# Optimization experiments

Hardware: AMD Instinct MI355X
Metric: run time of the kernel (lower is better)

## Reference

```python
import jax, jax.numpy as jnp
import numpy as np

B, SC, SV = 32, 300, 300
D, H, L, E, F = 512, 8, 6, 6, 1024
SEM = 768
VF = SEM + 1 + 1 + 6  # semantic + scene_offset + motion + emotion(6) = 776
CHORD, ROOT, ATTR = 159, 14, 14


def _ln(x, g, b, eps=1e-5):
    m = x.mean(-1, keepdims=True)
    v = ((x - m) ** 2).mean(-1, keepdims=True)
    return (x - m) / jnp.sqrt(v + eps) * g + b


def _mha(q_in, kv_in, qkv_w, qkv_b, ow, ob, mask=None):
    d = q_in.shape[-1]
    hd = d // H
    q = (q_in @ qkv_w[:d].T + qkv_b[:d]).reshape(q_in.shape[0], q_in.shape[1], H, hd)
    k = (kv_in @ qkv_w[d:2 * d].T + qkv_b[d:2 * d]).reshape(kv_in.shape[0], kv_in.shape[1], H, hd)
    v = (kv_in @ qkv_w[2 * d:].T + qkv_b[2 * d:]).reshape(kv_in.shape[0], kv_in.shape[1], H, hd)
    s = jnp.einsum('bqhd,bkhd->bhqk', q, k) / jnp.sqrt(jnp.asarray(hd, q.dtype))
    if mask is not None:
        s = s + mask
    a = jax.nn.softmax(s, axis=-1)
    o = jnp.einsum('bhqk,bkhd->bqhd', a, v).reshape(q_in.shape)
    return o @ ow.T + ob


def _moe(x, gw, gb, w1, b1, w2, b2, w3, b3):
    # top-2 routing over E experts, SwiGLU experts (GLUExpert)
    probs = jax.nn.softmax(x @ gw.T + gb, axis=-1)  # [B,S,E]
    topv, topi = jax.lax.top_k(probs, 2)
    wts = topv / topv.sum(-1, keepdims=True)
    full = (jax.nn.one_hot(topi, E, dtype=x.dtype) * wts[..., None]).sum(-2)  # [B,S,E]
    h = jax.nn.silu(jnp.einsum('bsd,edf->bsef', x, w1) + b1) * (jnp.einsum('bsd,edf->bsef', x, w2) + b2)
    eo = jnp.einsum('bsef,efd->bsed', h, w3) + b3
    return jnp.einsum('bse,bsed->bsd', full, eo)


def reference(x, x_root, x_attr, fsem, fkey, fscene, fmotion, femotion, emb_root, emb_attr, w_chord, b_chord, w_vis, b_vis, pos_c, pos_v, enc_qkv_w, enc_qkv_b, enc_ow, enc_ob, enc_ln1_g, enc_ln1_b, enc_ln2_g, enc_ln2_b, enc_gw, enc_gb, enc_w1, enc_b1, enc_w2, enc_b2, enc_w3, enc_b3, enc_fg, enc_fb, dec_sqkv_w, dec_sqkv_b, dec_sow, dec_sob, dec_cqkv_w, dec_cqkv_b, dec_cow, dec_cob, dec_ln1_g, dec_ln1_b, dec_ln2_g, dec_ln2_b, dec_ln3_g, dec_ln3_b, dec_gw, dec_gb, dec_w1, dec_b1, dec_w2, dec_b2, dec_w3, dec_b3, dec_fg, dec_fb, wout, bout):
    Bq, S = x_root.shape
    xe = emb_root[x_root] + emb_attr[x_attr]  # chord root + attr embeddings
    keyp = jnp.broadcast_to(fkey[:, 0][:, None, None], (Bq, S, 1)).astype(xe.dtype)
    xf = jnp.concatenate([xe, keyp], -1) @ w_chord.T + b_chord
    vfc = jnp.concatenate([fsem, fscene[..., None], fmotion[..., None], femotion], -1)  # [B,Sv,VF]
    vf = vfc @ w_vis.T + b_vis
    xf = xf + pos_c[:S][None]
    vf = vf + pos_v[:vf.shape[1]][None]
    causal = jnp.where(jnp.tril(jnp.ones((S, S), bool)), 0.0, jnp.finfo(xf.dtype).min).astype(xf.dtype)
    # encoder (post-norm): self-attn -> add&norm -> MoE -> add&norm
    h = vf
    for i in range(L):
        a = _mha(h, h, enc_qkv_w[i], enc_qkv_b[i], enc_ow[i], enc_ob[i])
        h = _ln(h + a, enc_ln1_g[i], enc_ln1_b[i])
        m = _moe(h, enc_gw[i], enc_gb[i], enc_w1[i], enc_b1[i], enc_w2[i], enc_b2[i], enc_w3[i], enc_b3[i])
        h = _ln(h + m, enc_ln2_g[i], enc_ln2_b[i])
    mem = _ln(h, enc_fg, enc_fb)
    # decoder: masked self-attn, cross-attn, MoE, each add&norm
    h = xf
    for i in range(L):
        a = _mha(h, h, dec_sqkv_w[i], dec_sqkv_b[i], dec_sow[i], dec_sob[i], causal)
        h = _ln(h + a, dec_ln1_g[i], dec_ln1_b[i])
        c = _mha(h, mem, dec_cqkv_w[i], dec_cqkv_b[i], dec_cow[i], dec_cob[i])
        h = _ln(h + c, dec_ln2_g[i], dec_ln2_b[i])
        m = _moe(h, dec_gw[i], dec_gb[i], dec_w1[i], dec_b1[i], dec_w2[i], dec_b2[i], dec_w3[i], dec_b3[i])
        h = _ln(h + m, dec_ln3_g[i], dec_ln3_b[i])
    h = _ln(h, dec_fg, dec_fb)
    return h @ wout.T + bout


def setup_inputs():
    key = jax.random.key(0)
    ks = iter(jax.random.split(key, 256))
    def nrm(*s):
        return jax.random.normal(next(ks), s, jnp.float32) * 0.02
    d = {}
    d['x'] = jax.random.randint(next(ks), (B, SC), 0, CHORD)
    d['x_root'] = jax.random.randint(next(ks), (B, SC), 0, ROOT)
    d['x_attr'] = jax.random.randint(next(ks), (B, SC), 0, ATTR)
    d['fsem'] = jax.random.normal(next(ks), (B, SV, SEM), jnp.float32)
    d['fkey'] = jax.random.uniform(next(ks), (B, 1), jnp.float32)
    d['fscene'] = jax.random.uniform(next(ks), (B, SV), jnp.float32)
    d['fmotion'] = jax.random.uniform(next(ks), (B, SV), jnp.float32)
    d['femotion'] = jax.random.uniform(next(ks), (B, SV, 6), jnp.float32)
    d['emb_root'] = nrm(ROOT, D)
    d['emb_attr'] = nrm(ATTR, D)
    d['w_chord'] = nrm(D, D + 1)
    d['b_chord'] = jnp.zeros((D,), jnp.float32)
    d['w_vis'] = nrm(D, VF)
    d['b_vis'] = jnp.zeros((D,), jnp.float32)
    d['pos_c'] = nrm(SC, D)
    d['pos_v'] = nrm(SV, D)
    def attn_params(pfx_qkv, pfx_o):
        d[pfx_qkv + '_w'] = nrm(L, 3 * D, D)
        d[pfx_qkv + '_b'] = jnp.zeros((L, 3 * D), jnp.float32)
        d[pfx_o + 'w'] = nrm(L, D, D)
        d[pfx_o + 'b'] = jnp.zeros((L, D), jnp.float32)
    attn_params('enc_qkv', 'enc_o')
    attn_params('dec_sqkv', 'dec_so')
    attn_params('dec_cqkv', 'dec_co')
    def moe_params(pfx):
        d[pfx + 'gw'] = nrm(L, E, D)
        d[pfx + 'gb'] = jnp.zeros((L, E), jnp.float32)
        d[pfx + 'w1'] = nrm(L, E, D, F)
        d[pfx + 'b1'] = jnp.zeros((L, E, F), jnp.float32)
        d[pfx + 'w2'] = nrm(L, E, D, F)
        d[pfx + 'b2'] = jnp.zeros((L, E, F), jnp.float32)
        d[pfx + 'w3'] = nrm(L, E, F, D)
        d[pfx + 'b3'] = jnp.zeros((L, E, D), jnp.float32)
    moe_params('enc_')
    moe_params('dec_')
    for n in ['enc_ln1', 'enc_ln2', 'dec_ln1', 'dec_ln2', 'dec_ln3']:
        d[n + '_g'] = jnp.ones((L, D), jnp.float32)
        d[n + '_b'] = jnp.zeros((L, D), jnp.float32)
    d['enc_fg'] = jnp.ones((D,), jnp.float32)
    d['enc_fb'] = jnp.zeros((D,), jnp.float32)
    d['dec_fg'] = jnp.ones((D,), jnp.float32)
    d['dec_fb'] = jnp.zeros((D,), jnp.float32)
    d['wout'] = nrm(CHORD, D)
    d['bout'] = jnp.zeros((CHORD,), jnp.float32)
    return d
```

## Files before the change

### kernel.cpp

```cpp
#include <hip/hip_runtime.h>

constexpr int B_ = 32, S_ = 300, D_ = 512, H_ = 8;
constexpr int L_ = 6, E_ = 6, F_ = 1024;
constexpr int CHORD_ = 159;
constexpr int R_ = B_ * S_;
constexpr int TD_ = 3 * D_;
constexpr int MT2_ = R_ / 128;
constexpr size_t WSCAP_ = (size_t)E_ * F_ * 512;

typedef short bfrag __attribute__((ext_vector_type(8)));
typedef float facc  __attribute__((ext_vector_type(4)));

static __device__ __forceinline__ facc mfma_(bfrag a, bfrag b, facc c) {
    return __builtin_amdgcn_mfma_f32_16x16x32_bf16(a, b, c, 0, 0, 0);
}

static __device__ __forceinline__ short f2bf_rne(float f) {
    unsigned u = __float_as_uint(f);
    return (short)((u + 0x7FFFu + ((u >> 16) & 1u)) >> 16);
}
static __device__ __forceinline__ void split2(float x, short& hi, short& lo) {
    unsigned u = __float_as_uint(x);
    hi = (short)(u >> 16);
    float fh = __uint_as_float(u & 0xFFFF0000u);
    lo = f2bf_rne(x - fh);
}

static __device__ __forceinline__ float2 blockReduce2(float s, float ss) {
    __shared__ float red[4][2];
    #pragma unroll
    for (int o = 32; o > 0; o >>= 1) { s += __shfl_down(s, o); ss += __shfl_down(ss, o); }
    const int wid = threadIdx.x >> 6, lane = threadIdx.x & 63;
    if (lane == 0) { red[wid][0] = s; red[wid][1] = ss; }
    __syncthreads();
    if (threadIdx.x == 0) {
        for (int w = 1; w < 4; ++w) { s += red[w][0]; ss += red[w][1]; }
        red[0][0] = s; red[0][1] = ss;
    }
    __syncthreads();
    return make_float2(red[0][0], red[0][1]);
}

__global__ void wsplit_kern(const float* __restrict__ src, short* __restrict__ dh, short* __restrict__ dl,
                            int N, int K, int Kp)
{
    const int idx = blockIdx.x * 256 + threadIdx.x;
    if (idx >= N * Kp) return;
    const int n = idx / Kp, k = idx - n * Kp;
    const float v = (k < K) ? src[(size_t)n * K + k] : 0.f;
    short sh, sl; split2(v, sh, sl);
    dh[idx] = sh; dl[idx] = sl;
}

__global__ __launch_bounds__(256) void tsplit_kern(const float* __restrict__ src,
                                                   short* __restrict__ dh, short* __restrict__ dl,
                                                   int K, int N)
{
    __shared__ float tile[32][33];
    const size_t eo = (size_t)blockIdx.z * K * N;
    const float* s = src + eo;
    short* oh = dh + eo;
    short* ol = dl + eo;
    const int kb = blockIdx.x * 32, nb = blockIdx.y * 32;
    const int c = threadIdx.x & 31, r0 = threadIdx.x >> 5;
    #pragma unroll
    for (int p = 0; p < 4; ++p) {
        const int r = r0 + p * 8;
        tile[r][c] = s[(size_t)(kb + r) * N + nb + c];
    }
    __syncthreads();
    #pragma unroll
    for (int p = 0; p < 4; ++p) {
        const int wn = r0 + p * 8;
        const float v = tile[c][wn];
        short sh, sl; split2(v, sh, sl);
        const size_t o = (size_t)(nb + wn) * K + kb + c;
        oh[o] = sh; ol[o] = sl;
    }
}

__global__ __launch_bounds__(256) void gemm_mfma(
    const short* __restrict__ Xh, const short* __restrict__ Xl,
    const short* __restrict__ Wh, const short* __restrict__ Wl, int Kp,
    const float* __restrict__ bias, const float* __restrict__ pos,
    float* __restrict__ Y, int ldy, int N,
    short* __restrict__ Yh, short* __restrict__ Yl)
{
    __shared__ __align__(16) short Ah[128][40], Al[128][40];
    __shared__ __align__(16) short Bh[128][40], Bl[128][40];
    const int m0 = blockIdx.x * 128, n0 = blockIdx.y * 128;
    const int tid = threadIdx.x;
    const int w = tid >> 6, l = tid & 63;
    const int wr = (w >> 1) * 64, wc = (w & 1) * 64;
    const facc zero = {0.f, 0.f, 0.f, 0.f};
    facc acc[4][4];
    #pragma unroll
    for (int i = 0; i < 4; ++i)
        #pragma unroll
        for (int j = 0; j < 4; ++j) acc[i][j] = zero;
    const int ar = tid >> 2, aks = (tid & 3) * 8;
    const int bc = tid >> 1, bk = (tid & 1) * 16;
    const bool bok = (n0 + bc) < N;
    const size_t a0 = (size_t)(m0 + ar) * Kp + aks;
    const size_t a1 = a0 + (size_t)64 * Kp;
    const size_t b0 = (size_t)(n0 + bc) * Kp + bk;
    const bfrag zf = {0, 0, 0, 0, 0, 0, 0, 0};
    bfrag pa0h, pa0l, pa1h, pa1l, pb0h, pb0l, pb1h, pb1l;
    auto LOAD = [&](int kc) {
        pa0h = *(const bfrag*)&Xh[a0 + kc];
        pa0l = *(const bfrag*)&Xl[a0 + kc];
        pa1h = *(const bfrag*)&Xh[a1 + kc];
        pa1l = *(const bfrag*)&Xl[a1 + kc];
        if (bok) {
            pb0h = *(const bfrag*)&Wh[b0 + kc];
            pb0l = *(const bfrag*)&Wl[b0 + kc];
            pb1h = *(const bfrag*)&Wh[b0 + kc + 8];
            pb1l = *(const bfrag*)&Wl[b0 + kc + 8];
        } else { pb0h = zf; pb0l = zf; pb1h = zf; pb1l = zf; }
    };
    LOAD(0);
    for (int kc = 0; kc < Kp; kc += 32) {
        *(bfrag*)&Ah[ar][aks]      = pa0h;  *(bfrag*)&Al[ar][aks]      = pa0l;
        *(bfrag*)&Ah[ar + 64][aks] = pa1h;  *(bfrag*)&Al[ar + 64][aks] = pa1l;
        *(bfrag*)&Bh[bc][bk]       = pb0h;  *(bfrag*)&Bl[bc][bk]       = pb0l;
        *(bfrag*)&Bh[bc][bk + 8]   = pb1h;  *(bfrag*)&Bl[bc][bk + 8]   = pb1l;
        __syncthreads();
        if (kc + 32 < Kp) LOAD(kc + 32);
        bfrag ah[4], al[4];
        #pragma unroll
        for (int i2 = 0; i2 < 4; ++i2) {
            ah[i2] = *(const bfrag*)&Ah[wr + i2 * 16 + (l & 15)][(l >> 4) * 8];
            al[i2] = *(const bfrag*)&Al[wr + i2 * 16 + (l & 15)][(l >> 4) * 8];
        }
        #pragma unroll
        for (int j = 0; j < 4; ++j) {
            const int cc = wc + j * 16 + (l & 15);
            const bfrag bh = *(const bfrag*)&Bh[cc][(l >> 4) * 8];
            const bfrag bl = *(const bfrag*)&Bl[cc][(l >> 4) * 8];
            #pragma unroll
            for (int i2 = 0; i2 < 4; ++i2) {
                acc[i2][j] = mfma_(ah[i2], bh, acc[i2][j]);
                acc[i2][j] = mfma_(al[i2], bh, acc[i2][j]);
                acc[i2][j] = mfma_(ah[i2], bl, acc[i2][j]);
            }
        }
        __syncthreads();
    }
    #pragma unroll
    for (int i2 = 0; i2 < 4; ++i2) {
        #pragma unroll
        for (int r = 0; r < 4; ++r) {
            const int m = m0 + wr + i2 * 16 + (l >> 4) * 4 + r;
            #pragma unroll
            for (int j = 0; j < 4; ++j) {
                const int n = n0 + wc + j * 16 + (l & 15);
                if (n < N) {
                    float y = acc[i2][j][r];
                    if (bias) y += bias[n];
                    if (pos)  y += pos[(size_t)(m % S_) * N + n];
                    Y[(size_t)m * ldy + n] = y;
                    if (Yh) {
                        short sh, sl; split2(y, sh, sl);
                        Yh[(size_t)m * ldy + n] = sh;
                        Yl[(size_t)m * ldy + n] = sl;
                    }
                }
            }
        }
    }
}

template<bool CAUSAL>
__global__ __launch_bounds__(320) void attn_kern(const float* __restrict__ qkv,
                                                 short* __restrict__ oh, short* __restrict__ ol)
{
    __shared__ float Ks[64][64];
    __shared__ float Vs[64][64];
    const int b = blockIdx.x >> 3, hh = blockIdx.x & 7;
    const int tid = threadIdx.x;
    const float* base = qkv + (size_t)b * S_ * TD_ + hh * 64;
    const bool act = tid < S_;
    float4 q4[16];
    if (act) {
        const float4* qp = (const float4*)(base + (size_t)tid * TD_);
        #pragma unroll
        for (int dd = 0; dd < 16; ++dd) q4[dd] = qp[dd];
    }
    float m = -3.0e38f, lsum = 0.f;
    float acc[64];
    #pragma unroll
    for (int d = 0; d < 64; ++d) acc[d] = 0.f;
    for (int j0 = 0; j0 < S_; j0 += 64) {
        const int tn = min(64, S_ - j0);
        __syncthreads();
        for (int idx = tid; idx < 64 * 64; idx += 320) {
            const int jj = idx >> 6, d = idx & 63;
            const bool ok = jj < tn;
            Ks[jj][d] = ok ? base[(size_t)(j0 + jj) * TD_ + D_ + d] : 0.f;
            Vs[jj][d] = ok ? base[(size_t)(j0 + jj) * TD_ + 2 * D_ + d] : 0.f;
        }
        __syncthreads();
        if (act) {
            const int jmax = CAUSAL ? min(tn, tid - j0 + 1) : tn;
            for (int jj = 0; jj < jmax; ++jj) {
                const float4* kp = (const float4*)Ks[jj];
                float s = 0.f;
                #pragma unroll
                for (int dd = 0; dd < 16; ++dd) {
                    const float4 kv = kp[dd];
                    s += q4[dd].x * kv.x + q4[dd].y * kv.y + q4[dd].z * kv.z + q4[dd].w * kv.w;
                }
                s *= 0.125f;
                float p;
                if (s > m) {
                    const float r = __expf(m - s);
                    lsum *= r;
                    #pragma unroll
                    for (int d = 0; d < 64; ++d) acc[d] *= r;
                    m = s; p = 1.f;
                } else {
                    p = __expf(s - m);
                }
                lsum += p;
                const float4* vp = (const float4*)Vs[jj];
                #pragma unroll
                for (int dd = 0; dd < 16; ++dd) {
                    const float4 vv = vp[dd];
                    acc[dd * 4 + 0] += p * vv.x; acc[dd * 4 + 1] += p * vv.y;
                    acc[dd * 4 + 2] += p * vv.z; acc[dd * 4 + 3] += p * vv.w;
                }
            }
        }
    }
    if (act) {
        const float inv = 1.f / lsum;
        const size_t ob = (size_t)(b * S_ + tid) * D_ + hh * 64;
        #pragma unroll
        for (int d = 0; d < 64; ++d) {
            short sh, sl; split2(acc[d] * inv, sh, sl);
            oh[ob + d] = sh; ol[ob + d] = sl;
        }
    }
}

__global__ __launch_bounds__(256) void add_ln_kern(float* __restrict__ h, const float* __restrict__ a,
    const float* __restrict__ g, const float* __restrict__ bb,
    short* __restrict__ dh, short* __restrict__ dl)
{
    const int r = blockIdx.x, tid = threadIdx.x;
    const size_t off = (size_t)r * D_;
    const float x0 = h[off + tid] + a[off + tid];
    const float x1 = h[off + tid + 256] + a[off + tid + 256];
    const float2 red = blockReduce2(x0 + x1, x0 * x0 + x1 * x1);
    const float mean = red.x * (1.f / D_);
    const float var = red.y * (1.f / D_) - mean * mean;
    const float rs = rsqrtf(var + 1e-5f);
    const float y0 = (x0 - mean) * rs * g[tid] + bb[tid];
    const float y1 = (x1 - mean) * rs * g[tid + 256] + bb[tid + 256];
    h[off + tid] = y0; h[off + tid + 256] = y1;
    short sh, sl;
    split2(y0, sh, sl); dh[off + tid] = sh;       dl[off + tid] = sl;
    split2(y1, sh, sl); dh[off + tid + 256] = sh; dl[off + tid + 256] = sl;
}

__global__ __launch_bounds__(256) void add2_ln_kern(float* __restrict__ h, const float* __restrict__ moeout,
    const float* __restrict__ g, const float* __restrict__ bb,
    short* __restrict__ dh, short* __restrict__ dl)
{
    const int r = blockIdx.x, tid = threadIdx.x;
    const size_t off = (size_t)r * D_;
    const size_t m0 = (size_t)(2 * r) * D_, m1 = (size_t)(2 * r + 1) * D_;
    const float x0 = h[off + tid]       + moeout[m0 + tid]       + moeout[m1 + tid];
    const float x1 = h[off + tid + 256] + moeout[m0 + tid + 256] + moeout[m1 + tid + 256];
    const float2 red = blockReduce2(x0 + x1, x0 * x0 + x1 * x1);
    const float mean = red.x * (1.f / D_);
    const float var = red.y * (1.f / D_) - mean * mean;
    const float rs = rsqrtf(var + 1e-5f);
    const float y0 = (x0 - mean) * rs * g[tid] + bb[tid];
    const float y1 = (x1 - mean) * rs * g[tid + 256] + bb[tid + 256];
    h[off + tid] = y0; h[off + tid + 256] = y1;
    short sh, sl;
    split2(y0, sh, sl); dh[off + tid] = sh;       dl[off + tid] = sl;
    split2(y1, sh, sl); dh[off + tid + 256] = sh; dl[off + tid + 256] = sl;
}

__global__ __launch_bounds__(256) void ln_kern(const float* __restrict__ src,
    const float* __restrict__ g, const float* __restrict__ bb,
    short* __restrict__ dh, short* __restrict__ dl)
{
    const int r = blockIdx.x, tid = threadIdx.x;
    const size_t off = (size_t)r * D_;
    const float x0 = src[off + tid];
    const float x1 = src[off + tid + 256];
    const float2 red = blockReduce2(x0 + x1, x0 * x0 + x1 * x1);
    const float mean = red.x * (1.f / D_);
    const float var = red.y * (1.f / D_) - mean * mean;
    const float rs = rsqrtf(var + 1e-5f);
    const float y0 = (x0 - mean) * rs * g[tid] + bb[tid];
    const float y1 = (x1 - mean) * rs * g[tid + 256] + bb[tid + 256];
    short sh, sl;
    split2(y0, sh, sl); dh[off + tid] = sh;       dl[off + tid] = sl;
    split2(y1, sh, sl); dh[off + tid + 256] = sh; dl[off + tid + 256] = sl;
}

__global__ void assemble_chord_split(const int* __restrict__ x_root, const int* __restrict__ x_attr,
    const float* __restrict__ emb_root, const float* __restrict__ emb_attr,
    const float* __restrict__ fkey, short* __restrict__ dh, short* __restrict__ dl)
{
    const int idx = blockIdx.x * 256 + threadIdx.x;
    if (idx >= R_ * 544) return;
    const int r = idx / 544, k = idx - r * 544;
    float v = 0.f;
    if (k < D_)       v = emb_root[x_root[r] * D_ + k] + emb_attr[x_attr[r] * D_ + k];
    else if (k == D_) v = fkey[r / S_];
    short sh, sl; split2(v, sh, sl);
    dh[idx] = sh; dl[idx] = sl;
}

__global__ void assemble_vis_split(const float* __restrict__ fsem, const float* __restrict__ fscene,
    const float* __restrict__ fmotion, const float* __restrict__ femotion,
    short* __restrict__ dh, short* __restrict__ dl)
{
    const int idx = blockIdx.x * 256 + threadIdx.x;
    if (idx >= R_ * 800) return;
    const int r = idx / 800, k = idx - r * 800;
    float v = 0.f;
    if (k < 768)       v = fsem[(size_t)r * 768 + k];
    else if (k == 768) v = fscene[r];
    else if (k == 769) v = fmotion[r];
    else if (k < 776)  v = femotion[(size_t)r * 6 + (k - 770)];
    short sh, sl; split2(v, sh, sl);
    dh[idx] = sh; dl[idx] = sl;
}

__global__ __launch_bounds__(256) void moe_route(const float* __restrict__ X,
    const float* __restrict__ gw, const float* __restrict__ gb,
    int* __restrict__ gcnt, int* __restrict__ gtok, float* __restrict__ gwt)
{
    const int t = blockIdx.x * 256 + threadIdx.x;
    if (t >= R_) return;
    float lg[E_];
    #pragma unroll
    for (int e = 0; e < E_; ++e) lg[e] = gb[e];
    const float* xp = X + (size_t)t * D_;
    for (int d = 0; d < D_; ++d) {
        const float xd = xp[d];
        #pragma unroll
        for (int e = 0; e < E_; ++e) lg[e] += xd * gw[e * D_ + d];
    }
    float mx = lg[0];
    #pragma unroll
    for (int e = 1; e < E_; ++e) mx = fmaxf(mx, lg[e]);
    float p[E_];
    #pragma unroll
    for (int e = 0; e < E_; ++e) p[e] = __expf(lg[e] - mx);
    int i1 = 0;
    #pragma unroll
    for (int e = 1; e < E_; ++e) if (p[e] > p[i1]) i1 = e;
    int i2 = (i1 == 0) ? 1 : 0;
    #pragma unroll
    for (int e = 0; e < E_; ++e) if (e != i1 && p[e] > p[i2]) i2 = e;
    const float denom = p[i1] + p[i2];
    const float w1 = p[i1] / denom, w2 = p[i2] / denom;
    int pos1 = atomicAdd(&gcnt[i1], 1);
    gtok[i1 * R_ + pos1] = t * 2;     gwt[i1 * R_ + pos1] = w1;
    int pos2 = atomicAdd(&gcnt[i2], 1);
    gtok[i2 * R_ + pos2] = t * 2 + 1; gwt[i2 * R_ + pos2] = w2;
}

__global__ __launch_bounds__(256) void moe_stageA(
    const short* __restrict__ Xh, const short* __restrict__ Xl,
    const short* __restrict__ W1h, const short* __restrict__ W1l,
    const short* __restrict__ W2h, const short* __restrict__ W2l,
    const float* __restrict__ b1, const float* __restrict__ b2,
    const int* __restrict__ gcnt, const int* __restrict__ gtok,
    short* __restrict__ H1h, short* __restrict__ H1l)
{
    const int e = blockIdx.x / MT2_, mt = blockIdx.x % MT2_;
    const int cnt = gcnt[e];
    const int m0t = mt * 128;
    if (m0t >= cnt) return;
    __shared__ int rid[128];
    __shared__ __align__(16) short Ah[128][40], Al[128][40];
    __shared__ __align__(16) short B1h[64][40], B1l[64][40], B2h[64][40], B2l[64][40];
    const int tid = threadIdx.x;
    if (tid < 128) rid[tid] = (m0t + tid < cnt) ? gtok[e * R_ + m0t + tid] : -1;
    __syncthreads();
    const int f0 = blockIdx.y * 64;
    const int w = tid >> 6, l = tid & 63;
    const int wr = (w >> 1) * 64, wf = (w & 1) * 32;
    const facc zero = {0.f, 0.f, 0.f, 0.f};
    facc acc1[4][2], acc2[4][2];
    #pragma unroll
    for (int i = 0; i < 4; ++i)
        #pragma unroll
        for (int j = 0; j < 2; ++j) { acc1[i][j] = zero; acc2[i][j] = zero; }
    const int ar = tid >> 2, aks = (tid & 3) * 8;
    const int r0 = rid[ar], r1 = rid[ar + 64];
    const size_t a0 = (r0 >= 0) ? ((size_t)(r0 >> 1) * 512 + aks) : 0;
    const size_t a1 = (r1 >= 0) ? ((size_t)(r1 >> 1) * 512 + aks) : 0;
    const int c = l;
    const short* bsrc = (w == 0) ? W1h : (w == 1) ? W1l : (w == 2) ? W2h : W2l;
    bsrc += ((size_t)e * F_ + f0 + c) * 512;
    short (*bdst)[40] = (w == 0) ? B1h : (w == 1) ? B1l : (w == 2) ? B2h : B2l;
    const bfrag zf = {0, 0, 0, 0, 0, 0, 0, 0};
    bfrag pa0h, pa0l, pa1h, pa1l, pb0, pb1, pb2, pb3;
    auto LOAD = [&](int kc) {
        pa0h = (r0 >= 0) ? *(const bfrag*)&Xh[a0 + kc] : zf;
        pa0l = (r0 >= 0) ? *(const bfrag*)&Xl[a0 + kc] : zf;
        pa1h = (r1 >= 0) ? *(const bfrag*)&Xh[a1 + kc] : zf;
        pa1l = (r1 >= 0) ? *(const bfrag*)&Xl[a1 + kc] : zf;
        pb0 = *(const bfrag*)&bsrc[kc];
        pb1 = *(const bfrag*)&bsrc[kc + 8];
        pb2 = *(const bfrag*)&bsrc[kc + 16];
        pb3 = *(const bfrag*)&bsrc[kc + 24];
    };
    LOAD(0);
    for (int kc = 0; kc < 512; kc += 32) {
        *(bfrag*)&Ah[ar][aks]      = pa0h;  *(bfrag*)&Al[ar][aks]      = pa0l;
        *(bfrag*)&Ah[ar + 64][aks] = pa1h;  *(bfrag*)&Al[ar + 64][aks] = pa1l;
        *(bfrag*)&bdst[c][0]  = pb0;  *(bfrag*)&bdst[c][8]  = pb1;
        *(bfrag*)&bdst[c][16] = pb2;  *(bfrag*)&bdst[c][24] = pb3;
        __syncthreads();
        if (kc + 32 < 512) LOAD(kc + 32);
        bfrag ah[4], al[4];
        #pragma unroll
        for (int i2 = 0; i2 < 4; ++i2) {
            ah[i2] = *(const bfrag*)&Ah[wr + i2 * 16 + (l & 15)][(l >> 4) * 8];
            al[i2] = *(const bfrag*)&Al[wr + i2 * 16 + (l & 15)][(l >> 4) * 8];
        }
        #pragma unroll
        for (int j = 0; j < 2; ++j) {
            const int fc = wf + j * 16 + (l & 15);
            const bfrag b1hf = *(const bfrag*)&B1h[fc][(l >> 4) * 8];
            const bfrag b1lf = *(const bfrag*)&B1l[fc][(l >> 4) * 8];
            const bfrag b2hf = *(const bfrag*)&B2h[fc][(l >> 4) * 8];
            const bfrag b2lf = *(const bfrag*)&B2l[fc][(l >> 4) * 8];
            #pragma unroll
            for (int i2 = 0; i2 < 4; ++i2) {
                acc1[i2][j] = mfma_(ah[i2], b1hf, acc1[i2][j]);
                acc1[i2][j] = mfma_(al[i2], b1hf, acc1[i2][j]);
                acc1[i2][j] = mfma_(ah[i2], b1lf, acc1[i2][j]);
                acc2[i2][j] = mfma_(ah[i2], b2hf, acc2[i2][j]);
                acc2[i2][j] = mfma_(al[i2], b2hf, acc2[i2][j]);
                acc2[i2][j] = mfma_(ah[i2], b2lf, acc2[i2][j]);
            }
        }
        __syncthreads();
    }
    #pragma unroll
    for (int i2 = 0; i2 < 4; ++i2) {
        #pragma unroll
        for (int r = 0; r < 4; ++r) {
            const int mi = wr + i2 * 16 + (l >> 4) * 4 + r;
            const int rr = rid[mi];
            if (rr < 0) continue;
            #pragma unroll
            for (int j = 0; j < 2; ++j) {
                const int f = f0 + wf + j * 16 + (l & 15);
                const float a1v = acc1[i2][j][r] + b1[e * F_ + f];
                const float a2v = acc2[i2][j][r] + b2[e * F_ + f];
                const float hv = (a1v / (1.f + __expf(-a1v))) * a2v;
                const size_t oi = (size_t)rr * F_ + f;
                short hs, ls; split2(hv, hs, ls);
                H1h[oi] = hs; H1l[oi] = ls;
            }
        }
    }
}

__global__ __launch_bounds__(256) void moe_stageB(
    const short* __restrict__ Xh, const short* __restrict__ Xl,
    const short* __restrict__ W3h, const short* __restrict__ W3l,
    const float* __restrict__ b3,
    const int* __restrict__ gcnt, const int* __restrict__ gtok, const float* __restrict__ gwt,
    float* __restrict__ moeout)
{
    const int e = blockIdx.x / MT2_, mt = blockIdx.x % MT2_;
    const int cnt = gcnt[e];
    const int m0t = mt * 128;
    if (m0t >= cnt) return;
    __shared__ int rid[128];
    __shared__ float wts[128];
    __shared__ __align__(16) short Ah[128][40], Al[128][40];
    __shared__ __align__(16) short Bh[128][40], Bl[128][40];
    const int tid = threadIdx.x;
    if (tid < 128) {
        rid[tid] = (m0t + tid < cnt) ? gtok[e * R_ + m0t + tid] : -1;
        wts[tid] = (m0t + tid < cnt) ? gwt[e * R_ + m0t + tid] : 0.f;
    }
    __syncthreads();
    const int n0 = blockIdx.y * 128;
    const int w = tid >> 6, l = tid & 63;
    const int wr = (w >> 1) * 64, wc = (w & 1) * 64;
    const facc zero = {0.f, 0.f, 0.f, 0.f};
    facc acc[4][4];
    #pragma unroll
    for (int i = 0; i < 4; ++i)
        #pragma unroll
        for (int j = 0; j < 4; ++j) acc[i][j] = zero;
    const int ar = tid >> 2, aks = (tid & 3) * 8;
    const int r0 = rid[ar], r1 = rid[ar + 64];
    const size_t a0 = (r0 >= 0) ? ((size_t)r0 * F_ + aks) : 0;
    const size_t a1 = (r1 >= 0) ? ((size_t)r1 * F_ + aks) : 0;
    const int bc = tid >> 1, bk = (tid & 1) * 16;
    const size_t b0 = ((size_t)e * 512 + n0 + bc) * 1024 + bk;
    const bfrag zf = {0, 0, 0, 0, 0, 0, 0, 0};
    bfrag pa0h, pa0l, pa1h, pa1l, pb0h, pb0l, pb1h, pb1l;
    auto LOAD = [&](int kc) {
        pa0h = (r0 >= 0) ? *(const bfrag*)&Xh[a0 + kc] : zf;
        pa0l = (r0 >= 0) ? *(const bfrag*)&Xl[a0 + kc] : zf;
        pa1h = (r1 >= 0) ? *(const bfrag*)&Xh[a1 + kc] : zf;
        pa1l = (r1 >= 0) ? *(const bfrag*)&Xl[a1 + kc] : zf;
        pb0h = *(const bfrag*)&W3h[b0 + kc];
        pb0l = *(const bfrag*)&W3l[b0 + kc];
        pb1h = *(const bfrag*)&W3h[b0 + kc + 8];
        pb1l = *(const bfrag*)&W3l[b0 + kc + 8];
    };
    LOAD(0);
    for (int kc = 0; kc < 1024; kc += 32) {
        *(bfrag*)&Ah[ar][aks]      = pa0h;  *(bfrag*)&Al[ar][aks]      = pa0l;
        *(bfrag*)&Ah[ar + 64][aks] = pa1h;  *(bfrag*)&Al[ar + 64][aks] = pa1l;
        *(bfrag*)&Bh[bc][bk]       = pb0h;  *(bfrag*)&Bl[bc][bk]       = pb0l;
        *(bfrag*)&Bh[bc][bk + 8]   = pb1h;  *(bfrag*)&Bl[bc][bk + 8]   = pb1l;
        __syncthreads();
        if (kc + 32 < 1024) LOAD(kc + 32);
        bfrag ah[4], al[4];
        #pragma unroll
        for (int i2 = 0; i2 < 4; ++i2) {
            ah[i2] = *(const bfrag*)&Ah[wr + i2 * 16 + (l & 15)][(l >> 4) * 8];
            al[i2] = *(const bfrag*)&Al[wr + i2 * 16 + (l & 15)][(l >> 4) * 8];
        }
        #pragma unroll
        for (int j = 0; j < 4; ++j) {
            const int cc = wc + j * 16 + (l & 15);
            const bfrag bh = *(const bfrag*)&Bh[cc][(l >> 4) * 8];
            const bfrag bl = *(const bfrag*)&Bl[cc][(l >> 4) * 8];
            #pragma unroll
            for (int i2 = 0; i2 < 4; ++i2) {
                acc[i2][j] = mfma_(ah[i2], bh, acc[i2][j]);
                acc[i2][j] = mfma_(al[i2], bh, acc[i2][j]);
                acc[i2][j] = mfma_(ah[i2], bl, acc[i2][j]);
            }
        }
        __syncthreads();
    }
    #pragma unroll
    for (int i2 = 0; i2 < 4; ++i2) {
        #pragma unroll
        for (int r = 0; r < 4; ++r) {
            const int mi = wr + i2 * 16 + (l >> 4) * 4 + r;
            const int rr = rid[mi];
            if (rr < 0) continue;
            const float wt = wts[mi];
            #pragma unroll
            for (int j = 0; j < 4; ++j) {
                const int n = n0 + wc + j * 16 + (l & 15);
                moeout[(size_t)rr * D_ + n] = wt * (acc[i2][j][r] + b3[e * D_ + n]);
            }
        }
    }
}

extern "C" void kernel_launch(void* const* d_in, const int* in_sizes, int n_in,
                              void* d_out, int out_size, void* d_ws, size_t ws_size,
                              hipStream_t stream) {
    (void)in_sizes; (void)n_in; (void)out_size; (void)ws_size;
    const int*   x_root    = (const int*)  d_in[1];
    const int*   x_attr    = (const int*)  d_in[2];
    const float* fsem      = (const float*)d_in[3];
    const float* fkey      = (const float*)d_in[4];
    const float* fscene    = (const float*)d_in[5];
    const float* fmotion   = (const float*)d_in[6];
    const float* femotion  = (const float*)d_in[7];
    const float* emb_root  = (const float*)d_in[8];
    const float* emb_attr  = (const float*)d_in[9];
    const float* w_chord   = (const float*)d_in[10];
    const float* b_chord   = (const float*)d_in[11];
    const float* w_vis     = (const float*)d_in[12];
    const float* b_vis     = (const float*)d_in[13];
    const float* pos_c     = (const float*)d_in[14];
    const float* pos_v     = (const float*)d_in[15];
    const float* enc_qkv_w = (const float*)d_in[16];
    const float* enc_qkv_b = (const float*)d_in[17];
    const float* enc_ow    = (const float*)d_in[18];
    const float* enc_ob    = (const float*)d_in[19];
    const float* dec_sqkv_w= (const float*)d_in[20];
    const float* dec_sqkv_b= (const float*)d_in[21];
    const float* dec_sow   = (const float*)d_in[22];
    const float* dec_sob   = (const float*)d_in[23];
    const float* dec_cqkv_w= (const float*)d_in[24];
    const float* dec_cqkv_b= (const float*)d_in[25];
    const float* dec_cow   = (const float*)d_in[26];
    const float* dec_cob   = (const float*)d_in[27];
    const float* enc_gw    = (const float*)d_in[28];
    const float* enc_gb    = (const float*)d_in[29];
    const float* enc_w1    = (const float*)d_in[30];
    const float* enc_b1    = (const float*)d_in[31];
    const float* enc_w2    = (const float*)d_in[32];
    const float* enc_b2    = (const float*)d_in[33];
    const float* enc_w3    = (const float*)d_in[34];
    const float* enc_b3    = (const float*)d_in[35];
    const float* dec_gw    = (const float*)d_in[36];
    const float* dec_gb    = (const float*)d_in[37];
    const float* dec_w1    = (const float*)d_in[38];
    const float* dec_b1    = (const float*)d_in[39];
    const float* dec_w2    = (const float*)d_in[40];
    const float* dec_b2    = (const float*)d_in[41];
    const float* dec_w3    = (const float*)d_in[42];
    const float* dec_b3    = (const float*)d_in[43];
    const float* enc_ln1_g = (const float*)d_in[44];
    const float* enc_ln1_b = (const float*)d_in[45];
    const float* enc_ln2_g = (const float*)d_in[46];
    const float* enc_ln2_b = (const float*)d_in[47];
    const float* dec_ln1_g = (const float*)d_in[48];
    const float* dec_ln1_b = (const float*)d_in[49];
    const float* dec_ln2_g = (const float*)d_in[50];
    const float* dec_ln2_b = (const float*)d_in[51];
    const float* dec_ln3_g = (const float*)d_in[52];
    const float* dec_ln3_b = (const float*)d_in[53];
    const float* enc_fg    = (const float*)d_in[54];
    const float* enc_fb    = (const float*)d_in[55];
    const float* dec_fg    = (const float*)d_in[56];
    const float* dec_fb    = (const float*)d_in[57];
    const float* wout      = (const float*)d_in[58];
    const float* bout      = (const float*)d_in[59];

    float* h    = (float*)d_ws;
    float* qkvb = h + (size_t)R_ * D_;
    short* PH   = (short*)(qkvb + (size_t)R_ * TD_);
    short* PL   = PH + (size_t)R_ * D_;
    short* MH   = PL + (size_t)R_ * D_;
    short* ML   = MH + (size_t)R_ * D_;
    short* H1H  = ML + (size_t)R_ * D_;
    short* H1L  = H1H + (size_t)2 * R_ * F_;
    short* WS0H = H1L + (size_t)2 * R_ * F_;
    short* WS0L = WS0H + WSCAP_;
    short* WS1H = WS0L + WSCAP_;
    short* WS1L = WS1H + WSCAP_;
    int*   gcnt = (int*)(WS1L + WSCAP_);
    int*   gtok = gcnt + 16;
    float* gwt  = (float*)(gtok + E_ * R_);
    short* AH   = (short*)qkvb;
    short* AL   = AH + (size_t)R_ * 800;

    auto wsplit = [&](const float* src, short* dh, short* dl, int N, int K, int Kp) {
        const int total = N * Kp;
        wsplit_kern<<<dim3((total + 255) / 256), dim3(256), 0, stream>>>(src, dh, dl, N, K, Kp);
    };
    auto tsplit = [&](const float* src, short* dh, short* dl, int K, int N) {
        tsplit_kern<<<dim3(K / 32, N / 32, E_), dim3(256), 0, stream>>>(src, dh, dl, K, N);
    };
    auto gemm = [&](const short* XhP, const short* XlP, int Kp,
                    const short* WhP, const short* WlP,
                    const float* bias, const float* pos,
                    float* Yf, int ldy, int N, short* Yh, short* Yl) {
        gemm_mfma<<<dim3(R_ / 128, (N + 127) / 128), dim3(256), 0, stream>>>(
            XhP, XlP, WhP, WlP, Kp, bias, pos, Yf, ldy, N, Yh, Yl);
    };
    auto run_moe = [&](const float* gw, const float* gb,
                       const float* w1, const float* b1, const float* w2, const float* b2,
                       const float* w3, const float* b3, const float* lng, const float* lnb) {
        hipMemsetAsync(gcnt, 0, 16 * sizeof(int), stream);
        moe_route<<<dim3((R_ + 255) / 256), dim3(256), 0, stream>>>(h, gw, gb, gcnt, gtok, gwt);
        tsplit(w1, WS0H, WS0L, D_, F_);
        tsplit(w2, WS1H, WS1L, D_, F_);
        moe_stageA<<<dim3(E_ * MT2_, F_ / 64), dim3(256), 0, stream>>>(
            PH, PL, WS0H, WS0L, WS1H, WS1L, b1, b2, gcnt, gtok, H1H, H1L);
        tsplit(w3, WS0H, WS0L, F_, D_);
        moe_stageB<<<dim3(E_ * MT2_, D_ / 128), dim3(256), 0, stream>>>(
            H1H, H1L, WS0H, WS0L, b3, gcnt, gtok, gwt, qkvb);
        add2_ln_kern<<<dim3(R_), dim3(256), 0, stream>>>(h, qkvb, lng, lnb, PH, PL);
    };

    wsplit(w_vis, WS0H, WS0L, D_, 776, 800);
    assemble_vis_split<<<dim3((R_ * 800 + 255) / 256), dim3(256), 0, stream>>>(
        fsem, fscene, fmotion, femotion, AH, AL);
    gemm(AH, AL, 800, WS0H, WS0L, b_vis, pos_v, h, D_, D_, PH, PL);

    for (int i = 0; i < L_; ++i) {
        wsplit(enc_qkv_w + (size_t)i * TD_ * D_, WS0H, WS0L, TD_, D_, D_);
        gemm(PH, PL, D_, WS0H, WS0L, enc_qkv_b + (size_t)i * TD_, nullptr, qkvb, TD_, TD_, nullptr, nullptr);
        attn_kern<false><<<dim3(B_ * H_), dim3(320), 0, stream>>>(qkvb, PH, PL);
        wsplit(enc_ow + (size_t)i * D_ * D_, WS0H, WS0L, D_, D_, D_);
        gemm(PH, PL, D_, WS0H, WS0L, enc_ob + (size_t)i * D_, nullptr, qkvb, D_, D_, nullptr, nullptr);
        add_ln_kern<<<dim3(R_), dim3(256), 0, stream>>>(h, qkvb, enc_ln1_g + i * D_, enc_ln1_b + i * D_, PH, PL);
        run_moe(enc_gw + (size_t)i * E_ * D_, enc_gb + (size_t)i * E_,
                enc_w1 + (size_t)i * E_ * D_ * F_, enc_b1 + (size_t)i * E_ * F_,
                enc_w2 + (size_t)i * E_ * D_ * F_, enc_b2 + (size_t)i * E_ * F_,
                enc_w3 + (size_t)i * E_ * F_ * D_, enc_b3 + (size_t)i * E_ * D_,
                enc_ln2_g + i * D_, enc_ln2_b + i * D_);
    }
    ln_kern<<<dim3(R_), dim3(256), 0, stream>>>(h, enc_fg, enc_fb, MH, ML);

    wsplit(w_chord, WS0H, WS0L, D_, 513, 544);
    assemble_chord_split<<<dim3((R_ * 544 + 255) / 256), dim3(256), 0, stream>>>(
        x_root, x_attr, emb_root, emb_attr, fkey, AH, AL);
    gemm(AH, AL, 544, WS0H, WS0L, b_chord, pos_c, h, D_, D_, PH, PL);

    for (int i = 0; i < L_; ++i) {
        wsplit(dec_sqkv_w + (size_t)i * TD_ * D_, WS0H, WS0L, TD_, D_, D_);
        gemm(PH, PL, D_, WS0H, WS0L, dec_sqkv_b + (size_t)i * TD_, nullptr, qkvb, TD_, TD_, nullptr, nullptr);
        attn_kern<true><<<dim3(B_ * H_), dim3(320), 0, stream>>>(qkvb, PH, PL);
        wsplit(dec_sow + (size_t)i * D_ * D_, WS0H, WS0L, D_, D_, D_);
        gemm(PH, PL, D_, WS0H, WS0L, dec_sob + (size_t)i * D_, nullptr, qkvb, D_, D_, nullptr, nullptr);
        add_ln_kern<<<dim3(R_), dim3(256), 0, stream>>>(h, qkvb, dec_ln1_g + i * D_, dec_ln1_b + i * D_, PH, PL);
        wsplit(dec_cqkv_w + (size_t)i * TD_ * D_, WS0H, WS0L, TD_, D_, D_);
        gemm(PH, PL, D_, WS0H, WS0L, dec_cqkv_b + (size_t)i * TD_, nullptr, qkvb, TD_, D_, nullptr, nullptr);
        gemm(MH, ML, D_, WS0H + (size_t)D_ * D_, WS0L + (size_t)D_ * D_,
             dec_cqkv_b + (size_t)i * TD_ + D_, nullptr, qkvb + D_, TD_, 2 * D_, nullptr, nullptr);
        attn_kern<false><<<dim3(B_ * H_), dim3(320), 0, stream>>>(qkvb, PH, PL);
        wsplit(dec_cow + (size_t)i * D_ * D_, WS0H, WS0L, D_, D_, D_);
        gemm(PH, PL, D_, WS0H, WS0L, dec_cob + (size_t)i * D_, nullptr, qkvb, D_, D_, nullptr, nullptr);
        add_ln_kern<<<dim3(R_), dim3(256), 0, stream>>>(h, qkvb, dec_ln2_g + i * D_, dec_ln2_b + i * D_, PH, PL);
        run_moe(dec_gw + (size_t)i * E_ * D_, dec_gb + (size_t)i * E_,
                dec_w1 + (size_t)i * E_ * D_ * F_, dec_b1 + (size_t)i * E_ * F_,
                dec_w2 + (size_t)i * E_ * D_ * F_, dec_b2 + (size_t)i * E_ * F_,
                dec_w3 + (size_t)i * E_ * F_ * D_, dec_b3 + (size_t)i * E_ * D_,
                dec_ln3_g + i * D_, dec_ln3_b + i * D_);
    }

    ln_kern<<<dim3(R_), dim3(256), 0, stream>>>(h, dec_fg, dec_fb, PH, PL);
    wsplit(wout, WS0H, WS0L, CHORD_, D_, D_);
    gemm(PH, PL, D_, WS0H, WS0L, bout, nullptr, (float*)d_out, CHORD_, CHORD_, nullptr, nullptr);
}
```

Measured before the change: 12.81 ms.

## Use wave-per-row layernorm and routing, lazy softmax rescale, pad K dims

```diff
diff --git a/kernel.cpp b/kernel.cpp
--- a/kernel.cpp
+++ b/kernel.cpp
@@ -24,21 +24,6 @@
     hi = (short)(u >> 16);
     float fh = __uint_as_float(u & 0xFFFF0000u);
     lo = f2bf_rne(x - fh);
-}
-
-static __device__ __forceinline__ float2 blockReduce2(float s, float ss) {
-    __shared__ float red[4][2];
-    #pragma unroll
-    for (int o = 32; o > 0; o >>= 1) { s += __shfl_down(s, o); ss += __shfl_down(ss, o); }
-    const int wid = threadIdx.x >> 6, lane = threadIdx.x & 63;
-    if (lane == 0) { red[wid][0] = s; red[wid][1] = ss; }
-    __syncthreads();
-    if (threadIdx.x == 0) {
-        for (int w = 1; w < 4; ++w) { s += red[w][0]; ss += red[w][1]; }
-        red[0][0] = s; red[0][1] = ss;
-    }
-    __syncthreads();
-    return make_float2(red[0][0], red[0][1]);
 }
 
 __global__ void wsplit_kern(const float* __restrict__ src, short* __restrict__ dh, short* __restrict__ dl,
@@ -204,23 +189,22 @@
             const int jmax = CAUSAL ? min(tn, tid - j0 + 1) : tn;
             for (int jj = 0; jj < jmax; ++jj) {
                 const float4* kp = (const float4*)Ks[jj];
-                float s = 0.f;
+                float s0 = 0.f, s1 = 0.f, s2 = 0.f, s3 = 0.f;
                 #pragma unroll
                 for (int dd = 0; dd < 16; ++dd) {
                     const float4 kv = kp[dd];
-                    s += q4[dd].x * kv.x + q4[dd].y * kv.y + q4[dd].z * kv.z + q4[dd].w * kv.w;
+                    s0 += q4[dd].x * kv.x; s1 += q4[dd].y * kv.y;
+                    s2 += q4[dd].z * kv.z; s3 += q4[dd].w * kv.w;
                 }
-                s *= 0.125f;
-                float p;
-                if (s > m) {
+                const float s = ((s0 + s1) + (s2 + s3)) * 0.125f;
+                if (s > m + 8.f) {
                     const float r = __expf(m - s);
                     lsum *= r;
                     #pragma unroll
                     for (int d = 0; d < 64; ++d) acc[d] *= r;
-                    m = s; p = 1.f;
-                } else {
-                    p = __expf(s - m);
+                    m = s;
                 }
+                const float p = __expf(s - m);
                 lsum += p;
                 const float4* vp = (const float4*)Vs[jj];
                 #pragma unroll
@@ -243,64 +227,88 @@
     }
 }
 
+static __device__ __forceinline__ float2 waveReduce2(float s, float ss) {
+    #pragma unroll
+    for (int o = 32; o > 0; o >>= 1) { s += __shfl_down(s, o); ss += __shfl_down(ss, o); }
+    s = __shfl(s, 0); ss = __shfl(ss, 0);
+    return make_float2(s, ss);
+}
+
+static __device__ __forceinline__ void ln_body(const float4 a, const float4 b,
+    const float* __restrict__ g, const float* __restrict__ bb, int lane,
+    float* __restrict__ outf, short* __restrict__ dh, short* __restrict__ dl, size_t off)
+{
+    const float sum = a.x + a.y + a.z + a.w + b.x + b.y + b.z + b.w;
+    const float ssq = a.x*a.x + a.y*a.y + a.z*a.z + a.w*a.w + b.x*b.x + b.y*b.y + b.z*b.z + b.w*b.w;
+    const float2 red = waveReduce2(sum, ssq);
+    const float mean = red.x * (1.f / D_);
+    const float var = red.y * (1.f / D_) - mean * mean;
+    const float rs = rsqrtf(var + 1e-5f);
+    const float4 ga = *(const float4*)&g[lane * 8];
+    const float4 gb4 = *(const float4*)&g[lane * 8 + 4];
+    const float4 ba = *(const float4*)&bb[lane * 8];
+    const float4 bb4 = *(const float4*)&bb[lane * 8 + 4];
+    float y[8];
+    y[0] = (a.x - mean) * rs * ga.x + ba.x;  y[1] = (a.y - mean) * rs * ga.y + ba.y;
+    y[2] = (a.z - mean) * rs * ga.z + ba.z;  y[3] = (a.w - mean) * rs * ga.w + ba.w;
+    y[4] = (b.x - mean) * rs * gb4.x + bb4.x; y[5] = (b.y - mean) * rs * gb4.y + bb4.y;
+    y[6] = (b.z - mean) * rs * gb4.z + bb4.z; y[7] = (b.w - mean) * rs * gb4.w + bb4.w;
+    if (outf) {
+        *(float4*)&outf[off + lane * 8]     = make_float4(y[0], y[1], y[2], y[3]);
+        *(float4*)&outf[off + lane * 8 + 4] = make_float4(y[4], y[5], y[6], y[7]);
+    }
+    bfrag vh, vl;
+    #pragma unroll
+    for (int i = 0; i < 8; ++i) { short sh, sl; split2(y[i], sh, sl); vh[i] = sh; vl[i] = sl; }
+    *(bfrag*)&dh[off + lane * 8] = vh;
+    *(bfrag*)&dl[off + lane * 8] = vl;
+}
+
 __global__ __launch_bounds__(256) void add_ln_kern(float* __restrict__ h, const float* __restrict__ a,
     const float* __restrict__ g, const float* __restrict__ bb,
     short* __restrict__ dh, short* __restrict__ dl)
 {
-    const int r = blockIdx.x, tid = threadIdx.x;
+    const int wid = threadIdx.x >> 6, lane = threadIdx.x & 63;
+    const int r = blockIdx.x * 4 + wid;
     const size_t off = (size_t)r * D_;
-    const float x0 = h[off + tid] + a[off + tid];
-    const float x1 = h[off + tid + 256] + a[off + tid + 256];
-    const float2 red = blockReduce2(x0 + x1, x0 * x0 + x1 * x1);
-    const float mean = red.x * (1.f / D_);
-    const float var = red.y * (1.f / D_) - mean * mean;
-    const float rs = rsqrtf(var + 1e-5f);
-    const float y0 = (x0 - mean) * rs * g[tid] + bb[tid];
-    const float y1 = (x1 - mean) * rs * g[tid + 256] + bb[tid + 256];
-    h[off + tid] = y0; h[off + tid + 256] = y1;
-    short sh, sl;
-    split2(y0, sh, sl); dh[off + tid] = sh;       dl[off + tid] = sl;
-    split2(y1, sh, sl); dh[off + tid + 256] = sh; dl[off + tid + 256] = sl;
+    float4 xa = *(const float4*)&h[off + lane * 8];
+    float4 xb = *(const float4*)&h[off + lane * 8 + 4];
+    const float4 aa = *(const float4*)&a[off + lane * 8];
+    const float4 ab = *(const float4*)&a[off + lane * 8 + 4];
+    xa.x += aa.x; xa.y += aa.y; xa.z += aa.z; xa.w += aa.w;
+    xb.x += ab.x; xb.y += ab.y; xb.z += ab.z; xb.w += ab.w;
+    ln_body(xa, xb, g, bb, lane, h, dh, dl, off);
 }
 
 __global__ __launch_bounds__(256) void add2_ln_kern(float* __restrict__ h, const float* __restrict__ moeout,
     const float* __restrict__ g, const float* __restrict__ bb,
     short* __restrict__ dh, short* __restrict__ dl)
 {
-    const int r = blockIdx.x, tid = threadIdx.x;
+    const int wid = threadIdx.x >> 6, lane = threadIdx.x & 63;
+    const int r = blockIdx.x * 4 + wid;
     const size_t off = (size_t)r * D_;
     const size_t m0 = (size_t)(2 * r) * D_, m1 = (size_t)(2 * r + 1) * D_;
-    const float x0 = h[off + tid]       + moeout[m0 + tid]       + moeout[m1 + tid];
-    const float x1 = h[off + tid + 256] + moeout[m0 + tid + 256] + moeout[m1 + tid + 256];
-    const float2 red = blockReduce2(x0 + x1, x0 * x0 + x1 * x1);
-    const float mean = red.x * (1.f / D_);
-    const float var = red.y * (1.f / D_) - mean * mean;
-    const float rs = rsqrtf(var + 1e-5f);
-    const float y0 = (x0 - mean) * rs * g[tid] + bb[tid];
-    const float y1 = (x1 - mean) * rs * g[tid + 256] + bb[tid + 256];
-    h[off + tid] = y0; h[off + tid + 256] = y1;
-    short sh, sl;
-    split2(y0, sh, sl); dh[off + tid] = sh;       dl[off + tid] = sl;
-    split2(y1, sh, sl); dh[off + tid + 256] = sh; dl[off + tid + 256] = sl;
+    float4 xa = *(const float4*)&h[off + lane * 8];
+    float4 xb = *(const float4*)&h[off + lane * 8 + 4];
+    const float4 p0a = *(const float4*)&moeout[m0 + lane * 8];
+    const float4 p0b = *(const float4*)&moeout[m0 + lane * 8 + 4];
+    const float4 p1a = *(const float4*)&moeout[m1 + lane * 8];
+    const float4 p1b = *(const float4*)&moeout[m1 + lane * 8 + 4];
+    xa.x += p0a.x + p1a.x; xa.y += p0a.y + p1a.y; xa.z += p0a.z + p1a.z; xa.w += p0a.w + p1a.w;
+    xb.x += p0b.x + p1b.x; xb.y += p0b.y + p1b.y; xb.z += p0b.z + p1b.z; xb.w += p0b.w + p1b.w;
+    ln_body(xa, xb, g, bb, lane, h, dh, dl, off);
 }
 
 __global__ __launch_bounds__(256) void ln_kern(const float* __restrict__ src,
     const float* __restrict__ g, const float* __restrict__ bb,
     short* __restrict__ dh, short* __restrict__ dl)
 {
-    const int r = blockIdx.x, tid = threadIdx.x;
+    const int wid = threadIdx.x >> 6, lane = threadIdx.x & 63;
+    const int r = blockIdx.x * 4 + wid;
     const size_t off = (size_t)r * D_;
-    const float x0 = src[off + tid];
-    const float x1 = src[off + tid + 256];
-    const float2 red = blockReduce2(x0 + x1, x0 * x0 + x1 * x1);
-    const float mean = red.x * (1.f / D_);
-    const float var = red.y * (1.f / D_) - mean * mean;
-    const float rs = rsqrtf(var + 1e-5f);
-    const float y0 = (x0 - mean) * rs * g[tid] + bb[tid];
-    const float y1 = (x1 - mean) * rs * g[tid + 256] + bb[tid + 256];
-    short sh, sl;
-    split2(y0, sh, sl); dh[off + tid] = sh;       dl[off + tid] = sl;
-    split2(y1, sh, sl); dh[off + tid + 256] = sh; dl[off + tid + 256] = sl;
+    const float4 xa = *(const float4*)&src[off + lane * 8];
+    const float4 xb = *(const float4*)&src[off + lane * 8 + 4];
+    ln_body(xa, xb, g, bb, lane, nullptr, dh, dl, off);
 }
 
 __global__ void assemble_chord_split(const int* __restrict__ x_root, const int* __restrict__ x_attr,
@@ -308,8 +316,8 @@
     const float* __restrict__ fkey, short* __restrict__ dh, short* __restrict__ dl)
 {
     const int idx = blockIdx.x * 256 + threadIdx.x;
-    if (idx >= R_ * 544) return;
-    const int r = idx / 544, k = idx - r * 544;
+    if (idx >= R_ * 576) return;
+    const int r = idx / 576, k = idx - r * 576;
     float v = 0.f;
     if (k < D_)       v = emb_root[x_root[r] * D_ + k] + emb_attr[x_attr[r] * D_ + k];
     else if (k == D_) v = fkey[r / S_];
@@ -322,8 +330,8 @@
     short* __restrict__ dh, short* __restrict__ dl)
 {
     const int idx = blockIdx.x * 256 + threadIdx.x;
-    if (idx >= R_ * 800) return;
-    const int r = idx / 800, k = idx - r * 800;
+    if (idx >= R_ * 832) return;
+    const int r = idx / 832, k = idx - r * 832;
     float v = 0.f;
     if (k < 768)       v = fsem[(size_t)r * 768 + k];
     else if (k == 768) v = fscene[r];
@@ -337,35 +345,45 @@
     const float* __restrict__ gw, const float* __restrict__ gb,
     int* __restrict__ gcnt, int* __restrict__ gtok, float* __restrict__ gwt)
 {
-    const int t = blockIdx.x * 256 + threadIdx.x;
-    if (t >= R_) return;
-    float lg[E_];
-    #pragma unroll
-    for (int e = 0; e < E_; ++e) lg[e] = gb[e];
-    const float* xp = X + (size_t)t * D_;
-    for (int d = 0; d < D_; ++d) {
-        const float xd = xp[d];
-        #pragma unroll
-        for (int e = 0; e < E_; ++e) lg[e] += xd * gw[e * D_ + d];
-    }
-    float mx = lg[0];
-    #pragma unroll
-    for (int e = 1; e < E_; ++e) mx = fmaxf(mx, lg[e]);
-    float p[E_];
-    #pragma unroll
-    for (int e = 0; e < E_; ++e) p[e] = __expf(lg[e] - mx);
-    int i1 = 0;
-    #pragma unroll
-    for (int e = 1; e < E_; ++e) if (p[e] > p[i1]) i1 = e;
-    int i2 = (i1 == 0) ? 1 : 0;
-    #pragma unroll
-    for (int e = 0; e < E_; ++e) if (e != i1 && p[e] > p[i2]) i2 = e;
-    const float denom = p[i1] + p[i2];
-    const float w1 = p[i1] / denom, w2 = p[i2] / denom;
-    int pos1 = atomicAdd(&gcnt[i1], 1);
-    gtok[i1 * R_ + pos1] = t * 2;     gwt[i1 * R_ + pos1] = w1;
-    int pos2 = atomicAdd(&gcnt[i2], 1);
-    gtok[i2 * R_ + pos2] = t * 2 + 1; gwt[i2 * R_ + pos2] = w2;
+    const int wid = threadIdx.x >> 6, lane = threadIdx.x & 63;
+    const int t = blockIdx.x * 4 + wid;
+    const float4 xa = *(const float4*)&X[(size_t)t * D_ + lane * 8];
+    const float4 xb = *(const float4*)&X[(size_t)t * D_ + lane * 8 + 4];
+    float p6[E_];
+    #pragma unroll
+    for (int e = 0; e < E_; ++e) {
+        const float4 ga = *(const float4*)&gw[e * D_ + lane * 8];
+        const float4 gb4 = *(const float4*)&gw[e * D_ + lane * 8 + 4];
+        p6[e] = xa.x*ga.x + xa.y*ga.y + xa.z*ga.z + xa.w*ga.w
+              + xb.x*gb4.x + xb.y*gb4.y + xb.z*gb4.z + xb.w*gb4.w;
+    }
+    #pragma unroll
+    for (int o = 32; o > 0; o >>= 1)
+        #pragma unroll
+        for (int e = 0; e < E_; ++e) p6[e] += __shfl_down(p6[e], o);
+    if (lane == 0) {
+        float lg[E_];
+        #pragma unroll
+        for (int e = 0; e < E_; ++e) lg[e] = p6[e] + gb[e];
+        float mx = lg[0];
+        #pragma unroll
+        for (int e = 1; e < E_; ++e) mx = fmaxf(mx, lg[e]);
+        float p[E_];
+        #pragma unroll
+        for (int e = 0; e < E_; ++e) p[e] = __expf(lg[e] - mx);
+        int i1 = 0;
+        #pragma unroll
+        for (int e = 1; e < E_; ++e) if (p[e] > p[i1]) i1 = e;
+        int i2 = (i1 == 0) ? 1 : 0;
+        #pragma unroll
+        for (int e = 0; e < E_; ++e) if (e != i1 && p[e] > p[i2]) i2 = e;
+        const float denom = p[i1] + p[i2];
+        const float w1 = p[i1] / denom, w2 = p[i2] / denom;
+        int pos1 = atomicAdd(&gcnt[i1], 1);
+        gtok[i1 * R_ + pos1] = t * 2;     gwt[i1 * R_ + pos1] = w1;
+        int pos2 = atomicAdd(&gcnt[i2], 1);
+        gtok[i2 * R_ + pos2] = t * 2 + 1; gwt[i2 * R_ + pos2] = w2;
+    }
 }
 
 __global__ __launch_bounds__(256) void moe_stageA(
@@ -642,7 +660,7 @@
     int*   gtok = gcnt + 16;
     float* gwt  = (float*)(gtok + E_ * R_);
     short* AH   = (short*)qkvb;
-    short* AL   = AH + (size_t)R_ * 800;
+    short* AL   = AH + (size_t)R_ * 832;
 
     auto wsplit = [&](const float* src, short* dh, short* dl, int N, int K, int Kp) {
         const int total = N * Kp;
@@ -662,7 +680,7 @@
                        const float* w1, const float* b1, const float* w2, const float* b2,
                        const float* w3, const float* b3, const float* lng, const float* lnb) {
         hipMemsetAsync(gcnt, 0, 16 * sizeof(int), stream);
-        moe_route<<<dim3((R_ + 255) / 256), dim3(256), 0, stream>>>(h, gw, gb, gcnt, gtok, gwt);
+        moe_route<<<dim3(R_ / 4), dim3(256), 0, stream>>>(h, gw, gb, gcnt, gtok, gwt);
         tsplit(w1, WS0H, WS0L, D_, F_);
         tsplit(w2, WS1H, WS1L, D_, F_);
         moe_stageA<<<dim3(E_ * MT2_, F_ / 64), dim3(256), 0, stream>>>(
@@ -670,13 +688,13 @@
         tsplit(w3, WS0H, WS0L, F_, D_);
         moe_stageB<<<dim3(E_ * MT2_, D_ / 128), dim3(256), 0, stream>>>(
             H1H, H1L, WS0H, WS0L, b3, gcnt, gtok, gwt, qkvb);
-        add2_ln_kern<<<dim3(R_), dim3(256), 0, stream>>>(h, qkvb, lng, lnb, PH, PL);
+        add2_ln_kern<<<dim3(R_ / 4), dim3(256), 0, stream>>>(h, qkvb, lng, lnb, PH, PL);
     };
 
-    wsplit(w_vis, WS0H, WS0L, D_, 776, 800);
-    assemble_vis_split<<<dim3((R_ * 800 + 255) / 256), dim3(256), 0, stream>>>(
+    wsplit(w_vis, WS0H, WS0L, D_, 776, 832);
+    assemble_vis_split<<<dim3((R_ * 832 + 255) / 256), dim3(256), 0, stream>>>(
         fsem, fscene, fmotion, femotion, AH, AL);
-    gemm(AH, AL, 800, WS0H, WS0L, b_vis, pos_v, h, D_, D_, PH, PL);
+    gemm(AH, AL, 832, WS0H, WS0L, b_vis, pos_v, h, D_, D_, PH, PL);
 
     for (int i = 0; i < L_; ++i) {
         wsplit(enc_qkv_w + (size_t)i * TD_ * D_, WS0H, WS0L, TD_, D_, D_);
@@ -684,19 +702,19 @@
         attn_kern<false><<<dim3(B_ * H_), dim3(320), 0, stream>>>(qkvb, PH, PL);
         wsplit(enc_ow + (size_t)i * D_ * D_, WS0H, WS0L, D_, D_, D_);
         gemm(PH, PL, D_, WS0H, WS0L, enc_ob + (size_t)i * D_, nullptr, qkvb, D_, D_, nullptr, nullptr);
-        add_ln_kern<<<dim3(R_), dim3(256), 0, stream>>>(h, qkvb, enc_ln1_g + i * D_, enc_ln1_b + i * D_, PH, PL);
+        add_ln_kern<<<dim3(R_ / 4), dim3(256), 0, stream>>>(h, qkvb, enc_ln1_g + i * D_, enc_ln1_b + i * D_, PH, PL);
         run_moe(enc_gw + (size_t)i * E_ * D_, enc_gb + (size_t)i * E_,
                 enc_w1 + (size_t)i * E_ * D_ * F_, enc_b1 + (size_t)i * E_ * F_,
                 enc_w2 + (size_t)i * E_ * D_ * F_, enc_b2 + (size_t)i * E_ * F_,
                 enc_w3 + (size_t)i * E_ * F_ * D_, enc_b3 + (size_t)i * E_ * D_,
                 enc_ln2_g + i * D_, enc_ln2_b + i * D_);
     }
-    ln_kern<<<dim3(R_), dim3(256), 0, stream>>>(h, enc_fg, enc_fb, MH, ML);
-
-    wsplit(w_chord, WS0H, WS0L, D_, 513, 544);
-    assemble_chord_split<<<dim3((R_ * 544 + 255) / 256), dim3(256), 0, stream>>>(
+    ln_kern<<<dim3(R_ / 4), dim3(256), 0, stream>>>(h, enc_fg, enc_fb, MH, ML);
+
+    wsplit(w_chord, WS0H, WS0L, D_, 513, 576);
+    assemble_chord_split<<<dim3((R_ * 576 + 255) / 256), dim3(256), 0, stream>>>(
         x_root, x_attr, emb_root, emb_attr, fkey, AH, AL);
-    gemm(AH, AL, 544, WS0H, WS0L, b_chord, pos_c, h, D_, D_, PH, PL);
+    gemm(AH, AL, 576, WS0H, WS0L, b_chord, pos_c, h, D_, D_, PH, PL);
 
     for (int i = 0; i < L_; ++i) {
         wsplit(dec_sqkv_w + (size_t)i * TD_ * D_, WS0H, WS0L, TD_, D_, D_);
@@ -704,7 +722,7 @@
         attn_kern<true><<<dim3(B_ * H_), dim3(320), 0, stream>>>(qkvb, PH, PL);
         wsplit(dec_sow + (size_t)i * D_ * D_, WS0H, WS0L, D_, D_, D_);
         gemm(PH, PL, D_, WS0H, WS0L, dec_sob + (size_t)i * D_, nullptr, qkvb, D_, D_, nullptr, nullptr);
-        add_ln_kern<<<dim3(R_), dim3(256), 0, stream>>>(h, qkvb, dec_ln1_g + i * D_, dec_ln1_b + i * D_, PH, PL);
+        add_ln_kern<<<dim3(R_ / 4), dim3(256), 0, stream>>>(h, qkvb, dec_ln1_g + i * D_, dec_ln1_b + i * D_, PH, PL);
         wsplit(dec_cqkv_w + (size_t)i * TD_ * D_, WS0H, WS0L, TD_, D_, D_);
         gemm(PH, PL, D_, WS0H, WS0L, dec_cqkv_b + (size_t)i * TD_, nullptr, qkvb, TD_, D_, nullptr, nullptr);
         gemm(MH, ML, D_, WS0H + (size_t)D_ * D_, WS0L + (size_t)D_ * D_,
@@ -712,7 +730,7 @@
         attn_kern<false><<<dim3(B_ * H_), dim3(320), 0, stream>>>(qkvb, PH, PL);
         wsplit(dec_cow + (size_t)i * D_ * D_, WS0H, WS0L, D_, D_, D_);
         gemm(PH, PL, D_, WS0H, WS0L, dec_cob + (size_t)i * D_, nullptr, qkvb, D_, D_, nullptr, nullptr);
-        add_ln_kern<<<dim3(R_), dim3(256), 0, stream>>>(h, qkvb, dec_ln2_g + i * D_, dec_ln2_b + i * D_, PH, PL);
+        add_ln_kern<<<dim3(R_ / 4), dim3(256), 0, stream>>>(h, qkvb, dec_ln2_g + i * D_, dec_ln2_b + i * D_, PH, PL);
         run_moe(dec_gw + (size_t)i * E_ * D_, dec_gb + (size_t)i * E_,
                 dec_w1 + (size_t)i * E_ * D_ * F_, dec_b1 + (size_t)i * E_ * F_,
                 dec_w2 + (size_t)i * E_ * D_ * F_, dec_b2 + (size_t)i * E_ * F_,
@@ -720,7 +738,7 @@
                 dec_ln3_g + i * D_, dec_ln3_b + i * D_);
     }
 
-    ln_kern<<<dim3(R_), dim3(256), 0, stream>>>(h, dec_fg, dec_fb, PH, PL);
+    ln_kern<<<dim3(R_ / 4), dim3(256), 0, stream>>>(h, dec_fg, dec_fb, PH, PL);
     wsplit(wout, WS0H, WS0L, CHORD_, D_, D_);
     gemm(PH, PL, D_, WS0H, WS0L, bout, nullptr, (float*)d_out, CHORD_, CHORD_, nullptr, nullptr);
 }
```

After: 13.78 ms. 7.5% more time.
